# Optimization experiments

Measured on AMD Instinct MI355X. Metric: run time of the kernel, lower is better.

## Reference

```python
import jax, jax.numpy as jnp
import numpy as np

EPS = 1e-5


def _interp_conv(x, pos_in, pos_out, idx, w1, b1, w2, b2, kernel, bias):
    # x: [B, Cin, Nin]; idx: [Nout, K] neighbor indices into the input grid.
    off = pos_in[idx] - pos_out[:, None, :]            # [Nout, K, 2] relative offsets
    h = jax.nn.relu(off @ w1 + b1)                     # [Nout, K, 16] weight-net hidden
    A = h @ w2 + b2                                    # [Nout, K, T] interp weights onto T kernel taps
    feat = x[:, :, idx]                                # [B, Cin, Nout, K] irregular gather
    taps = jnp.einsum('bcnk,nkt->bcnt', feat, A)       # resample neighbors onto canonical taps
    return jnp.einsum('bcnt,oct->bon', taps, kernel) + bias[None, :, None]


def _bn_relu(x, g, b):
    # BatchNorm1d (training-style batch stats over (B, N)) + ReLU
    m = x.mean(axis=(0, 2), keepdims=True)
    v = x.var(axis=(0, 2), keepdims=True)
    return jax.nn.relu((x - m) * jax.lax.rsqrt(v + EPS) * g[None, :, None] + b[None, :, None])


def setup_inputs():
    key = jax.random.key(0)
    ks = jax.random.split(key, 24)
    B, N1, N2, N3, K, T = 16, 50176, 12544, 3136, 9, 9
    d = {}
    d['x'] = jax.random.normal(ks[0], (B, 3, N1), jnp.float32)
    d['l1'] = jax.random.uniform(ks[1], (N1, 2), jnp.float32)
    d['l2'] = jax.random.uniform(ks[2], (N2, 2), jnp.float32)
    d['l3'] = jax.random.uniform(ks[3], (N3, 2), jnp.float32)
    d['knn1'] = jax.random.randint(ks[4], (N2, K), 0, N1)
    d['knn2'] = jax.random.randint(ks[5], (N2, K), 0, N2)
    d['knn3'] = jax.random.randint(ks[6], (N2, K), 0, N2)
    d['pool_idx'] = jax.random.randint(ks[7], (N3, 4), 0, N2)
    cins = {'c1': 3, 'c2': 32, 'c3': 32}
    couts = {'c1': 32, 'c2': 32, 'c3': 64}
    for i, p in enumerate(['c1', 'c2', 'c3']):
        d[p + '_wn_w1'] = jax.random.normal(ks[8 + 4 * i], (2, 16), jnp.float32) * 0.5
        d[p + '_wn_b1'] = jnp.zeros(16, jnp.float32)
        d[p + '_wn_w2'] = jax.random.normal(ks[9 + 4 * i], (16, T), jnp.float32) * 0.3
        d[p + '_wn_b2'] = jnp.zeros(T, jnp.float32)
        d[p + '_kernel'] = jax.random.normal(ks[10 + 4 * i], (couts[p], cins[p], T), jnp.float32) * np.float32(1.0 / np.sqrt(cins[p] * T))
        d[p + '_bias'] = jnp.zeros(couts[p], jnp.float32)
    for p, c in [('bn1', 32), ('bn2', 32), ('bn3', 64)]:
        d[p + '_g'] = jnp.ones(c, jnp.float32)
        d[p + '_b'] = jnp.zeros(c, jnp.float32)
    return d


def reference(x, l1, l2, l3, knn1, knn2, knn3, pool_idx,
              c1_wn_w1, c1_wn_b1, c1_wn_w2, c1_wn_b2, c1_kernel, c1_bias,
              c2_wn_w1, c2_wn_b1, c2_wn_w2, c2_wn_b2, c2_kernel, c2_bias,
              c3_wn_w1, c3_wn_b1, c3_wn_w2, c3_wn_b2, c3_kernel, c3_bias,
              bn1_g, bn1_b, bn2_g, bn2_b, bn3_g, bn3_b):
    h = _interp_conv(x, l1, l2, knn1, c1_wn_w1, c1_wn_b1, c1_wn_w2, c1_wn_b2, c1_kernel, c1_bias)
    h = _bn_relu(h, bn1_g, bn1_b)
    h = _interp_conv(h, l2, l2, knn2, c2_wn_w1, c2_wn_b1, c2_wn_w2, c2_wn_b2, c2_kernel, c2_bias)
    h = _bn_relu(h, bn2_g, bn2_b)
    h = _interp_conv(h, l2, l2, knn3, c3_wn_w1, c3_wn_b1, c3_wn_w2, c3_wn_b2, c3_kernel, c3_bias)
    h = _bn_relu(h, bn3_g, bn3_b)
    # MaxPoolNG: max over 4 nearest neighbors on the non-uniform grid -> [B, 64, N3]
    return h[:, :, pool_idx].max(axis=-1)
```

## Files before the change

### kernel.cpp

```cpp
#include <hip/hip_runtime.h>
#include <hip/hip_bf16.h>
#include <cfloat>

#define N1C 50176
#define N2C 12544
#define N3C 3136

typedef __attribute__((ext_vector_type(8))) short short8v;
typedef __attribute__((ext_vector_type(4))) float f32x4;

static __device__ __forceinline__ unsigned short f2bf(float f){
  __hip_bfloat16 h = __float2bfloat16(f);
  return *reinterpret_cast<unsigned short*>(&h);
}
static __device__ __forceinline__ float bflo(unsigned v){
  return __uint_as_float(v << 16);
}
static __device__ __forceinline__ float bfhi(unsigned v){
  return __uint_as_float(v & 0xFFFF0000u);
}
static __device__ __forceinline__ float bf2f(unsigned short u){
  return __uint_as_float(((unsigned)u) << 16);
}
static __device__ __forceinline__ unsigned pk2(float a, float b){
  return (unsigned)f2bf(a) | ((unsigned)f2bf(b) << 16);
}
static __device__ __forceinline__ short8v pack8(f32x4 L, f32x4 H){
  short8v r;
  r[0]=(short)f2bf(L[0]); r[1]=(short)f2bf(L[1]); r[2]=(short)f2bf(L[2]); r[3]=(short)f2bf(L[3]);
  r[4]=(short)f2bf(H[0]); r[5]=(short)f2bf(H[1]); r[6]=(short)f2bf(H[2]); r[7]=(short)f2bf(H[3]);
  return r;
}

__global__ __launch_bounds__(256) void transpose_x_kernel(
    const float* __restrict__ x, unsigned short* __restrict__ xTb)
{
  __shared__ float tile[48][65];
  int n0 = blockIdx.x * 64;
  int tid = threadIdx.x;
  int i = tid & 63;
  for (int rr = tid >> 6; rr < 48; rr += 4)
    tile[rr][i] = x[(size_t)rr * N1C + n0 + i];
  __syncthreads();
  for (int j = tid; j < 64*64; j += 256){
    int ii = j >> 6, bc = j & 63, b = bc >> 2, c = bc & 3;
    float v = (c < 3) ? tile[b*3 + c][ii] : 0.f;
    xTb[(size_t)n0 * 64 + j] = f2bf(v);
  }
}

__global__ __launch_bounds__(256) void compute_A_kernel(
    const float* __restrict__ pos_in, const float* __restrict__ pos_out,
    const int* __restrict__ idx,
    const float* __restrict__ w1, const float* __restrict__ b1,
    const float* __restrict__ w2, const float* __restrict__ b2,
    float* __restrict__ Abuf)
{
  int g = blockIdx.x * 256 + threadIdx.x;
  if (g >= N2C * 9) return;
  int n = g / 9;
  int p = idx[g];
  float o0 = pos_in[2*p]   - pos_out[2*n];
  float o1 = pos_in[2*p+1] - pos_out[2*n+1];
  float A[9];
  #pragma unroll
  for (int t = 0; t < 9; t++) A[t] = b2[t];
  #pragma unroll
  for (int j = 0; j < 16; j++){
    float h = fmaxf(fmaf(o0, w1[j], fmaf(o1, w1[16+j], b1[j])), 0.f);
    #pragma unroll
    for (int t = 0; t < 9; t++) A[t] = fmaf(h, w2[j*9 + t], A[t]);
  }
  #pragma unroll
  for (int t = 0; t < 9; t++) Abuf[(size_t)g*9 + t] = A[t];
}

__global__ __launch_bounds__(256) void wcvt_kernel(
    const float* __restrict__ W, unsigned short* __restrict__ Wb,
    int total, int K, int KW, int mode)
{
  int i = blockIdx.x * 256 + threadIdx.x;
  if (i >= total) return;
  int o = i / KW, r = i % KW;
  float v;
  if (mode == 0){
    v = (r < K) ? W[o*K + r] : 0.f;
  } else {
    int t = r >> 5, c = r & 31;
    v = W[o*288 + c*9 + t];
  }
  Wb[i] = f2bf(v);
}

template<int CIN, int CINP, int COUT, int NPB, bool AFFINE>
__global__ __launch_bounds__(256) void conv_mfma_kernel(
    const unsigned short* __restrict__ in, const int* __restrict__ idx,
    const float* __restrict__ Abuf, const unsigned short* __restrict__ Wb,
    const float* __restrict__ bias,
    const float* __restrict__ scale, const float* __restrict__ shift,
    unsigned short* __restrict__ out, float* __restrict__ gpart)
{
  constexpr int K    = CIN * 9;
  constexpr int KW   = (K < 32) ? 32 : K;
  constexpr int KROW = (K < 32) ? 48 : 296;
  constexpr int CHUNKS = KW / 32;
  constexpr int OT   = COUT / 16;
  constexpr int HP   = CINP / 2;
  constexpr int PPT  = 16 * HP;

  __shared__ alignas(16) unsigned short Tb[NPB * 16 * KROW];
  __shared__ float As[NPB * 81];
  __shared__ int   Ip[NPB * 9];
  __shared__ float Sw[4 * COUT];
  __shared__ float Sq[4 * COUT];

  int n0 = blockIdx.x * NPB;
  int tid = threadIdx.x;
  for (int i = tid; i < NPB*81; i += 256) As[i] = Abuf[(size_t)n0*81 + i];
  if (tid < NPB*9) Ip[tid] = idx[n0*9 + tid];
  for (int i = tid; i < 4*COUT; i += 256){ Sw[i] = 0.f; Sq[i] = 0.f; }
  if (K < 32){
    for (int i = tid; i < NPB*16*KROW/2; i += 256) ((unsigned*)Tb)[i] = 0u;
  }
  __syncthreads();

  for (int u = tid; u < NPB*PPT; u += 256){
    int ni = u / PPT, loc = u % PPT;
    int b = loc / HP, c2 = loc % HP;
    const float* As_n = As + ni*81;
    const int*   ip   = Ip + ni*9;
    float scx=1.f, shx=0.f, scy=1.f, shy=0.f;
    if (AFFINE){
      scx = scale[2*c2];   shx = shift[2*c2];
      scy = scale[2*c2+1]; shy = shift[2*c2+1];
    }
    float fx[9], fy[9];
    #pragma unroll
    for (int k = 0; k < 9; k++){
      unsigned v = *(const unsigned*)(in + ((size_t)ip[k]*16 + b)*CINP + 2*c2);
      float x0 = bflo(v), y0 = bfhi(v);
      if (AFFINE){
        x0 = fmaxf(fmaf(x0, scx, shx), 0.f);
        y0 = fmaxf(fmaf(y0, scy, shy), 0.f);
      }
      fx[k] = x0; fy[k] = y0;
    }
    unsigned short e[18];
    #pragma unroll
    for (int t = 0; t < 9; t++){
      float s0 = 0.f, s1 = 0.f;
      #pragma unroll
      for (int k = 0; k < 9; k++){
        float a = As_n[k*9 + t];
        s0 = fmaf(fx[k], a, s0);
        s1 = fmaf(fy[k], a, s1);
      }
      e[t] = f2bf(s0); e[9+t] = f2bf(s1);
    }
    unsigned* dst = (unsigned*)(Tb + (ni*16 + b)*KROW + 18*c2);
    #pragma unroll
    for (int j = 0; j < 9; j++) dst[j] = (unsigned)e[2*j] | ((unsigned)e[2*j+1] << 16);
  }
  __syncthreads();

  int w = tid >> 6, l = tid & 63, lr = l & 15, lg = l >> 4;
  float smr[4] = {0,0,0,0}, sqr[4] = {0,0,0,0};
  int oBase = 0;
  for (int wi = w; wi < NPB*OT; wi += 4){
    int ni = wi / OT, ot = wi % OT;
    oBase = 16*ot + 4*lg;
    f32x4 acc;
    #pragma unroll
    for (int r = 0; r < 4; r++) acc[r] = bias[oBase + r];
    const short8v* ap = (const short8v*)(Wb + (size_t)(16*ot + lr)*KW) + lg;
    const short8v* bp = (const short8v*)(Tb + (ni*16 + lr)*KROW) + lg;
    #pragma unroll
    for (int kk = 0; kk < CHUNKS; kk++)
      acc = __builtin_amdgcn_mfma_f32_16x16x32_bf16(ap[kk*4], bp[kk*4], acc, 0, 0, 0);
    ushort4 o4;
    o4.x = f2bf(acc[0]); o4.y = f2bf(acc[1]); o4.z = f2bf(acc[2]); o4.w = f2bf(acc[3]);
    *(ushort4*)(out + ((size_t)(n0 + ni)*16 + lr)*COUT + oBase) = o4;
    #pragma unroll
    for (int r = 0; r < 4; r++){
      smr[r] += acc[r];
      sqr[r] = fmaf(acc[r], acc[r], sqr[r]);
    }
  }
  #pragma unroll
  for (int m = 1; m < 16; m <<= 1){
    #pragma unroll
    for (int r = 0; r < 4; r++){
      smr[r] += __shfl_xor(smr[r], m);
      sqr[r] += __shfl_xor(sqr[r], m);
    }
  }
  if (lr == 0){
    #pragma unroll
    for (int r = 0; r < 4; r++){
      Sw[w*COUT + oBase + r] = smr[r];
      Sq[w*COUT + oBase + r] = sqr[r];
    }
  }
  __syncthreads();
  for (int o = tid; o < COUT; o += 256){
    float sm = Sw[o] + Sw[COUT + o] + Sw[2*COUT + o] + Sw[3*COUT + o];
    float sq = Sq[o] + Sq[COUT + o] + Sq[2*COUT + o] + Sq[3*COUT + o];
    gpart[(size_t)blockIdx.x * 2*COUT + o] = sm;
    gpart[(size_t)blockIdx.x * 2*COUT + COUT + o] = sq;
  }
}

template<int COUT>
__global__ __launch_bounds__(256, 2) void conv_wave_kernel(
    const unsigned short* __restrict__ in, const int* __restrict__ idx,
    const float* __restrict__ Abuf, const unsigned short* __restrict__ Wb,
    const float* __restrict__ bias,
    const float* __restrict__ scale, const float* __restrict__ shift,
    unsigned short* __restrict__ out, float* __restrict__ gpart)
{
  constexpr int NPB = 4;
  constexpr int OT  = COUT / 16;
  constexpr int USZ = 128;

  __shared__ alignas(16) float U[NPB * USZ];

  int tid = threadIdx.x;
  int w = tid >> 6, l = tid & 63;
  int n0 = blockIdx.x * NPB;
  int nws = __builtin_amdgcn_readfirstlane(n0 + w);

  const float* Ap = Abuf + (size_t)nws * 81;
  float a0 = Ap[l];
  float a1 = (l < 17) ? Ap[64 + l] : 0.f;

  int ip[9];
  {
    const int* ipr = idx + nws * 9;
    #pragma unroll
    for (int k = 0; k < 9; k++) ip[k] = ipr[k];
  }

  int b = l & 15, cg = l >> 4;
  const unsigned short* gbase = in + b*32 + cg*8;
  uint4 rv0 = *(const uint4*)(gbase + (size_t)ip[0]*512);
  uint4 rv1 = *(const uint4*)(gbase + (size_t)ip[1]*512);
  uint4 rv2 = *(const uint4*)(gbase + (size_t)ip[2]*512);
  uint4 rv3 = *(const uint4*)(gbase + (size_t)ip[3]*512);
  uint4 rv4 = *(const uint4*)(gbase + (size_t)ip[4]*512);
  uint4 rv5 = *(const uint4*)(gbase + (size_t)ip[5]*512);
  uint4 rv6 = *(const uint4*)(gbase + (size_t)ip[6]*512);
  uint4 rv7 = *(const uint4*)(gbase + (size_t)ip[7]*512);
  uint4 rv8 = *(const uint4*)(gbase + (size_t)ip[8]*512);
  float4 scLf = *(const float4*)(scale + cg*8);
  float4 scHf = *(const float4*)(scale + cg*8 + 4);
  float4 shLf = *(const float4*)(shift + cg*8);
  float4 shHf = *(const float4*)(shift + cg*8 + 4);
  __builtin_amdgcn_sched_barrier(0);

  float* Aw = U + w * USZ;
  {
    int k = l / 9, t = l - k*9;
    Aw[k*12 + t] = a0;
    if (l < 17){
      int j = l + 64;
      int k2 = j / 9, t2 = j - k2*9;
      Aw[k2*12 + t2] = a1;
    }
  }

  f32x4 scL; scL[0]=scLf.x; scL[1]=scLf.y; scL[2]=scLf.z; scL[3]=scLf.w;
  f32x4 shL; shL[0]=shLf.x; shL[1]=shLf.y; shL[2]=shLf.z; shL[3]=shLf.w;
  f32x4 scH; scH[0]=scHf.x; scH[1]=scHf.y; scH[2]=scHf.z; scH[3]=scHf.w;
  f32x4 shH; shH[0]=shHf.x; shH[1]=shHf.y; shH[2]=shHf.z; shH[3]=shHf.w;

  f32x4 tL0={0,0,0,0},tL1={0,0,0,0},tL2={0,0,0,0},tL3={0,0,0,0},tL4={0,0,0,0},
        tL5={0,0,0,0},tL6={0,0,0,0},tL7={0,0,0,0},tL8={0,0,0,0};
  f32x4 tH0={0,0,0,0},tH1={0,0,0,0},tH2={0,0,0,0},tH3={0,0,0,0},tH4={0,0,0,0},
        tH5={0,0,0,0},tH6={0,0,0,0},tH7={0,0,0,0},tH8={0,0,0,0};

#define KSTEP(RV, K) { \
    f32x4 fL_, fH_; \
    fL_[0]=bflo(RV.x); fL_[1]=bfhi(RV.x); fL_[2]=bflo(RV.y); fL_[3]=bfhi(RV.y); \
    fH_[0]=bflo(RV.z); fH_[1]=bfhi(RV.z); fH_[2]=bflo(RV.w); fH_[3]=bfhi(RV.w); \
    fL_ = fL_ * scL + shL; fH_ = fH_ * scH + shH; \
    fL_[0]=fmaxf(fL_[0],0.f); fL_[1]=fmaxf(fL_[1],0.f); \
    fL_[2]=fmaxf(fL_[2],0.f); fL_[3]=fmaxf(fL_[3],0.f); \
    fH_[0]=fmaxf(fH_[0],0.f); fH_[1]=fmaxf(fH_[1],0.f); \
    fH_[2]=fmaxf(fH_[2],0.f); fH_[3]=fmaxf(fH_[3],0.f); \
    f32x4 a03_ = *(const f32x4*)(Aw + (K)*12); \
    f32x4 a47_ = *(const f32x4*)(Aw + (K)*12 + 4); \
    float a8_ = Aw[(K)*12 + 8]; \
    tL0 += fL_ * a03_[0]; tH0 += fH_ * a03_[0]; \
    tL1 += fL_ * a03_[1]; tH1 += fH_ * a03_[1]; \
    tL2 += fL_ * a03_[2]; tH2 += fH_ * a03_[2]; \
    tL3 += fL_ * a03_[3]; tH3 += fH_ * a03_[3]; \
    tL4 += fL_ * a47_[0]; tH4 += fH_ * a47_[0]; \
    tL5 += fL_ * a47_[1]; tH5 += fH_ * a47_[1]; \
    tL6 += fL_ * a47_[2]; tH6 += fH_ * a47_[2]; \
    tL7 += fL_ * a47_[3]; tH7 += fH_ * a47_[3]; \
    tL8 += fL_ * a8_;     tH8 += fH_ * a8_; }

  KSTEP(rv0,0) KSTEP(rv1,1) KSTEP(rv2,2) KSTEP(rv3,3) KSTEP(rv4,4)
  KSTEP(rv5,5) KSTEP(rv6,6) KSTEP(rv7,7) KSTEP(rv8,8)
#undef KSTEP

  short8v fr0 = pack8(tL0, tH0);
  short8v fr1 = pack8(tL1, tH1);
  short8v fr2 = pack8(tL2, tH2);
  short8v fr3 = pack8(tL3, tH3);
  short8v fr4 = pack8(tL4, tH4);
  short8v fr5 = pack8(tL5, tH5);
  short8v fr6 = pack8(tL6, tH6);
  short8v fr7 = pack8(tL7, tH7);
  short8v fr8 = pack8(tL8, tH8);

  f32x4 sm0={0,0,0,0}, sm1={0,0,0,0}, sm2={0,0,0,0}, sm3={0,0,0,0};
  f32x4 sq0={0,0,0,0}, sq1={0,0,0,0}, sq2={0,0,0,0}, sq3={0,0,0,0};
  #pragma unroll
  for (int ot = 0; ot < OT; ot++){
    int oBase = 16*ot + 4*cg;
    f32x4 a3;
    a3[0]=bias[oBase]; a3[1]=bias[oBase+1]; a3[2]=bias[oBase+2]; a3[3]=bias[oBase+3];
    const short8v* ap = (const short8v*)(Wb + (size_t)(16*ot + b)*288) + cg;
    a3 = __builtin_amdgcn_mfma_f32_16x16x32_bf16(ap[0],  fr0, a3, 0, 0, 0);
    a3 = __builtin_amdgcn_mfma_f32_16x16x32_bf16(ap[4],  fr1, a3, 0, 0, 0);
    a3 = __builtin_amdgcn_mfma_f32_16x16x32_bf16(ap[8],  fr2, a3, 0, 0, 0);
    a3 = __builtin_amdgcn_mfma_f32_16x16x32_bf16(ap[12], fr3, a3, 0, 0, 0);
    a3 = __builtin_amdgcn_mfma_f32_16x16x32_bf16(ap[16], fr4, a3, 0, 0, 0);
    a3 = __builtin_amdgcn_mfma_f32_16x16x32_bf16(ap[20], fr5, a3, 0, 0, 0);
    a3 = __builtin_amdgcn_mfma_f32_16x16x32_bf16(ap[24], fr6, a3, 0, 0, 0);
    a3 = __builtin_amdgcn_mfma_f32_16x16x32_bf16(ap[28], fr7, a3, 0, 0, 0);
    a3 = __builtin_amdgcn_mfma_f32_16x16x32_bf16(ap[32], fr8, a3, 0, 0, 0);
    ushort4 o4;
    o4.x = f2bf(a3[0]); o4.y = f2bf(a3[1]); o4.z = f2bf(a3[2]); o4.w = f2bf(a3[3]);
    *(ushort4*)(out + ((size_t)nws*16 + b)*COUT + oBase) = o4;
    if (ot==0){ sm0 += a3; sq0 += a3*a3; }
    else if (ot==1){ sm1 += a3; sq1 += a3*a3; }
    else if (ot==2){ sm2 += a3; sq2 += a3*a3; }
    else { sm3 += a3; sq3 += a3*a3; }
  }

  #pragma unroll
  for (int ot = 0; ot < OT; ot++){
    f32x4 s = (ot==0) ? sm0 : ((ot==1) ? sm1 : ((ot==2) ? sm2 : sm3));
    f32x4 q = (ot==0) ? sq0 : ((ot==1) ? sq1 : ((ot==2) ? sq2 : sq3));
    #pragma unroll
    for (int m = 1; m < 16; m <<= 1){
      #pragma unroll
      for (int r = 0; r < 4; r++){
        s[r] += __shfl_xor(s[r], m);
        q[r] += __shfl_xor(q[r], m);
      }
    }
    if (b == 0){
      int oBase = 16*ot + 4*cg;
      #pragma unroll
      for (int r = 0; r < 4; r++){
        U[w*USZ + oBase + r]        = s[r];
        U[w*USZ + COUT + oBase + r] = q[r];
      }
    }
  }
  __syncthreads();
  for (int o = tid; o < COUT; o += 256){
    float smv = U[o] + U[USZ + o] + U[2*USZ + o] + U[3*USZ + o];
    float sqv = U[COUT + o] + U[USZ + COUT + o] + U[2*USZ + COUT + o] + U[3*USZ + COUT + o];
    gpart[(size_t)blockIdx.x * 2*COUT + o] = smv;
    gpart[(size_t)blockIdx.x * 2*COUT + COUT + o] = sqv;
  }
}

__global__ __launch_bounds__(256) void bn_finalize_kernel(
    const float* __restrict__ gpart, int NB, int C,
    const float* __restrict__ g, const float* __restrict__ bb,
    float* __restrict__ sc, float* __restrict__ sh, float invN)
{
  int c = blockIdx.x;
  float sm = 0.f, sq = 0.f;
  for (int i = threadIdx.x; i < NB; i += 256){
    sm += gpart[(size_t)i*2*C + c];
    sq += gpart[(size_t)i*2*C + C + c];
  }
  #pragma unroll
  for (int off = 32; off > 0; off >>= 1){
    sm += __shfl_down(sm, off);
    sq += __shfl_down(sq, off);
  }
  __shared__ float rs[8];
  int wd = threadIdx.x >> 6, ln = threadIdx.x & 63;
  if (ln == 0){ rs[wd] = sm; rs[4+wd] = sq; }
  __syncthreads();
  if (threadIdx.x == 0){
    float S = rs[0]+rs[1]+rs[2]+rs[3], Q = rs[4]+rs[5]+rs[6]+rs[7];
    float mean = S * invN;
    float var  = fmaxf(Q * invN - mean*mean, 0.f);
    float s = g[c] * rsqrtf(var + 1e-5f);
    sc[c] = s;
    sh[c] = bb[c] - mean * s;
  }
}

__global__ __launch_bounds__(256) void pool_kernel(
    const unsigned short* __restrict__ h3, const int* __restrict__ pidx,
    const float* __restrict__ sc, const float* __restrict__ sh,
    float* __restrict__ out)
{
  __shared__ float P[16][1024];
  int m0 = blockIdx.x * 16;
  int tid = threadIdx.x;
  for (int mi = 0; mi < 16; mi++){
    int m = m0 + mi;
    int p0 = pidx[m*4+0], p1 = pidx[m*4+1], p2 = pidx[m*4+2], p3 = pidx[m*4+3];
    #pragma unroll
    for (int q = 0; q < 4; q++){
      int bo = tid + q*256;
      int o = bo & 63;
      float s = sc[o], h = sh[o];
      float v0 = fmaf(bf2f(h3[(size_t)p0*1024 + bo]), s, h);
      float v1 = fmaf(bf2f(h3[(size_t)p1*1024 + bo]), s, h);
      float v2 = fmaf(bf2f(h3[(size_t)p2*1024 + bo]), s, h);
      float v3 = fmaf(bf2f(h3[(size_t)p3*1024 + bo]), s, h);
      P[mi][bo] = fmaxf(fmaxf(fmaxf(v0,v1), fmaxf(v2,v3)), 0.f);
    }
  }
  __syncthreads();
  #pragma unroll
  for (int w = 0; w < 4; w++){
    int r = tid + w*256;
    float* dst = out + (size_t)r*N3C + m0;
    #pragma unroll
    for (int mi = 0; mi < 16; mi++) dst[mi] = P[mi][r];
  }
}

extern "C" void kernel_launch(void* const* d_in, const int* in_sizes, int n_in,
                              void* d_out, int out_size, void* d_ws, size_t ws_size,
                              hipStream_t stream)
{
  const float* x    = (const float*)d_in[0];
  const float* l1   = (const float*)d_in[1];
  const float* l2   = (const float*)d_in[2];
  const int* knn1   = (const int*)d_in[4];
  const int* knn2   = (const int*)d_in[5];
  const int* knn3   = (const int*)d_in[6];
  const int* pidx   = (const int*)d_in[7];

  const float* c1_w1 = (const float*)d_in[8];
  const float* c1_b1 = (const float*)d_in[9];
  const float* c1_w2 = (const float*)d_in[10];
  const float* c1_b2 = (const float*)d_in[11];
  const float* c1_k  = (const float*)d_in[12];
  const float* c1_bs = (const float*)d_in[13];
  const float* c2_w1 = (const float*)d_in[14];
  const float* c2_b1 = (const float*)d_in[15];
  const float* c2_w2 = (const float*)d_in[16];
  const float* c2_b2 = (const float*)d_in[17];
  const float* c2_k  = (const float*)d_in[18];
  const float* c2_bs = (const float*)d_in[19];
  const float* c3_w1 = (const float*)d_in[20];
  const float* c3_b1 = (const float*)d_in[21];
  const float* c3_w2 = (const float*)d_in[22];
  const float* c3_b2 = (const float*)d_in[23];
  const float* c3_k  = (const float*)d_in[24];
  const float* c3_bs = (const float*)d_in[25];
  const float* bn1_g = (const float*)d_in[26];
  const float* bn1_b = (const float*)d_in[27];
  const float* bn2_g = (const float*)d_in[28];
  const float* bn2_b = (const float*)d_in[29];
  const float* bn3_g = (const float*)d_in[30];
  const float* bn3_b = (const float*)d_in[31];

  char* ws = (char*)d_ws;
  unsigned short* xTb = (unsigned short*)(ws + 0);
  unsigned short* h1  = (unsigned short*)(ws + 6422528);
  unsigned short* h2  = (unsigned short*)(ws + 19267584);
  unsigned short* h3  = (unsigned short*)(ws + 32112640);
  float* Abuf         = (float*)(ws + 57802752);
  float* gpart        = (float*)(ws + 61867008);
  unsigned short* wb1 = (unsigned short*)(ws + 65078272);
  unsigned short* wb2 = (unsigned short*)(ws + 65081344);
  unsigned short* wb3 = (unsigned short*)(ws + 65099776);
  float* sc1 = (float*)(ws + 65137664); float* sh1 = sc1 + 32;
  float* sc2 = sh1 + 32;                float* sh2 = sc2 + 32;
  float* sc3 = sh2 + 32;                float* sh3 = sc3 + 64;

  const float invN = 1.0f / (float)(N2C * 16);
  const int ablocks = (N2C * 9 + 255) / 256;

  transpose_x_kernel<<<N1C/64, 256, 0, stream>>>(x, xTb);
  wcvt_kernel<<<(32*32 + 255)/256, 256, 0, stream>>>(c1_k, wb1, 32*32, 27, 32, 0);
  wcvt_kernel<<<(32*288 + 255)/256, 256, 0, stream>>>(c2_k, wb2, 32*288, 288, 288, 1);
  wcvt_kernel<<<(64*288 + 255)/256, 256, 0, stream>>>(c3_k, wb3, 64*288, 288, 288, 1);

  compute_A_kernel<<<ablocks, 256, 0, stream>>>(l1, l2, knn1, c1_w1, c1_b1, c1_w2, c1_b2, Abuf);
  conv_mfma_kernel<3, 4, 32, 8, false><<<N2C/8, 256, 0, stream>>>(
      xTb, knn1, Abuf, wb1, c1_bs, nullptr, nullptr, h1, gpart);
  bn_finalize_kernel<<<32, 256, 0, stream>>>(gpart, N2C/8, 32, bn1_g, bn1_b, sc1, sh1, invN);

  compute_A_kernel<<<ablocks, 256, 0, stream>>>(l2, l2, knn2, c2_w1, c2_b1, c2_w2, c2_b2, Abuf);
  conv_wave_kernel<32><<<N2C/4, 256, 0, stream>>>(
      h1, knn2, Abuf, wb2, c2_bs, sc1, sh1, h2, gpart);
  bn_finalize_kernel<<<32, 256, 0, stream>>>(gpart, N2C/4, 32, bn2_g, bn2_b, sc2, sh2, invN);

  compute_A_kernel<<<ablocks, 256, 0, stream>>>(l2, l2, knn3, c3_w1, c3_b1, c3_w2, c3_b2, Abuf);
  conv_wave_kernel<64><<<N2C/4, 256, 0, stream>>>(
      h2, knn3, Abuf, wb3, c3_bs, sc2, sh2, h3, gpart);
  bn_finalize_kernel<<<64, 256, 0, stream>>>(gpart, N2C/4, 64, bn3_g, bn3_b, sc3, sh3, invN);

  pool_kernel<<<N3C/16, 256, 0, stream>>>(h3, pidx, sc3, sh3, (float*)d_out);
}
```

Measured before the change: 171.1 us.

## Process four points per wave with software-pipelined gathers and LDS-staged weights

Each wave now handles four output points instead of one. The neighbor gather and A-weight loads for the next point are issued before the MFMA/stat stage of the current point, hiding gather latency. Conv weights are copied once per block into LDS with a padded row stride instead of being read from global per MFMA. This raises register and LDS use per block and cuts the block count by four, which may lower occupancy.

```diff
diff --git a/kernel.cpp b/kernel.cpp
--- a/kernel.cpp
+++ b/kernel.cpp
@@ -210,73 +210,25 @@
   }
 }
 
-template<int COUT>
-__global__ __launch_bounds__(256, 2) void conv_wave_kernel(
-    const unsigned short* __restrict__ in, const int* __restrict__ idx,
-    const float* __restrict__ Abuf, const unsigned short* __restrict__ Wb,
-    const float* __restrict__ bias,
-    const float* __restrict__ scale, const float* __restrict__ shift,
-    unsigned short* __restrict__ out, float* __restrict__ gpart)
-{
-  constexpr int NPB = 4;
-  constexpr int OT  = COUT / 16;
-  constexpr int USZ = 128;
-
-  __shared__ alignas(16) float U[NPB * USZ];
-
-  int tid = threadIdx.x;
-  int w = tid >> 6, l = tid & 63;
-  int n0 = blockIdx.x * NPB;
-  int nws = __builtin_amdgcn_readfirstlane(n0 + w);
-
-  const float* Ap = Abuf + (size_t)nws * 81;
-  float a0 = Ap[l];
-  float a1 = (l < 17) ? Ap[64 + l] : 0.f;
-
-  int ip[9];
-  {
-    const int* ipr = idx + nws * 9;
-    #pragma unroll
-    for (int k = 0; k < 9; k++) ip[k] = ipr[k];
-  }
-
-  int b = l & 15, cg = l >> 4;
-  const unsigned short* gbase = in + b*32 + cg*8;
-  uint4 rv0 = *(const uint4*)(gbase + (size_t)ip[0]*512);
-  uint4 rv1 = *(const uint4*)(gbase + (size_t)ip[1]*512);
-  uint4 rv2 = *(const uint4*)(gbase + (size_t)ip[2]*512);
-  uint4 rv3 = *(const uint4*)(gbase + (size_t)ip[3]*512);
-  uint4 rv4 = *(const uint4*)(gbase + (size_t)ip[4]*512);
-  uint4 rv5 = *(const uint4*)(gbase + (size_t)ip[5]*512);
-  uint4 rv6 = *(const uint4*)(gbase + (size_t)ip[6]*512);
-  uint4 rv7 = *(const uint4*)(gbase + (size_t)ip[7]*512);
-  uint4 rv8 = *(const uint4*)(gbase + (size_t)ip[8]*512);
-  float4 scLf = *(const float4*)(scale + cg*8);
-  float4 scHf = *(const float4*)(scale + cg*8 + 4);
-  float4 shLf = *(const float4*)(shift + cg*8);
-  float4 shHf = *(const float4*)(shift + cg*8 + 4);
-  __builtin_amdgcn_sched_barrier(0);
-
-  float* Aw = U + w * USZ;
-  {
-    int k = l / 9, t = l - k*9;
-    Aw[k*12 + t] = a0;
-    if (l < 17){
-      int j = l + 64;
-      int k2 = j / 9, t2 = j - k2*9;
-      Aw[k2*12 + t2] = a1;
-    }
-  }
-
-  f32x4 scL; scL[0]=scLf.x; scL[1]=scLf.y; scL[2]=scLf.z; scL[3]=scLf.w;
-  f32x4 shL; shL[0]=shLf.x; shL[1]=shLf.y; shL[2]=shLf.z; shL[3]=shLf.w;
-  f32x4 scH; scH[0]=scHf.x; scH[1]=scHf.y; scH[2]=scHf.z; scH[3]=scHf.w;
-  f32x4 shH; shH[0]=shHf.x; shH[1]=shHf.y; shH[2]=shHf.z; shH[3]=shHf.w;
-
-  f32x4 tL0={0,0,0,0},tL1={0,0,0,0},tL2={0,0,0,0},tL3={0,0,0,0},tL4={0,0,0,0},
-        tL5={0,0,0,0},tL6={0,0,0,0},tL7={0,0,0,0},tL8={0,0,0,0};
-  f32x4 tH0={0,0,0,0},tH1={0,0,0,0},tH2={0,0,0,0},tH3={0,0,0,0},tH4={0,0,0,0},
-        tH5={0,0,0,0},tH6={0,0,0,0},tH7={0,0,0,0},tH8={0,0,0,0};
+
+#define PREFETCH(NWSN) { \
+    const float* Ap_ = Abuf + (size_t)(NWSN)*81; \
+    a0 = Ap_[l]; a1 = (l < 17) ? Ap_[64 + l] : 0.f; \
+    const int* ipr_ = idx + (size_t)(NWSN)*9; \
+    int i0_=ipr_[0], i1_=ipr_[1], i2_=ipr_[2], i3_=ipr_[3], i4_=ipr_[4], \
+        i5_=ipr_[5], i6_=ipr_[6], i7_=ipr_[7], i8_=ipr_[8]; \
+    rv0 = *(const uint4*)(gbase + (size_t)i0_*512); \
+    rv1 = *(const uint4*)(gbase + (size_t)i1_*512); \
+    rv2 = *(const uint4*)(gbase + (size_t)i2_*512); \
+    rv3 = *(const uint4*)(gbase + (size_t)i3_*512); \
+    rv4 = *(const uint4*)(gbase + (size_t)i4_*512); \
+    rv5 = *(const uint4*)(gbase + (size_t)i5_*512); \
+    rv6 = *(const uint4*)(gbase + (size_t)i6_*512); \
+    rv7 = *(const uint4*)(gbase + (size_t)i7_*512); \
+    rv8 = *(const uint4*)(gbase + (size_t)i8_*512); }
+
+#define AWRITE { int k_ = l/9, t_ = l - k_*9; Aw[k_*12 + t_] = a0; \
+    if (l < 17){ int j_ = l + 64; int k2_ = j_/9, t2_ = j_ - k2_*9; Aw[k2_*12 + t2_] = a1; } }
 
 #define KSTEP(RV, K) { \
     f32x4 fL_, fH_; \
@@ -300,45 +252,115 @@
     tL7 += fL_ * a47_[3]; tH7 += fH_ * a47_[3]; \
     tL8 += fL_ * a8_;     tH8 += fH_ * a8_; }
 
-  KSTEP(rv0,0) KSTEP(rv1,1) KSTEP(rv2,2) KSTEP(rv3,3) KSTEP(rv4,4)
-  KSTEP(rv5,5) KSTEP(rv6,6) KSTEP(rv7,7) KSTEP(rv8,8)
-#undef KSTEP
-
-  short8v fr0 = pack8(tL0, tH0);
-  short8v fr1 = pack8(tL1, tH1);
-  short8v fr2 = pack8(tL2, tH2);
-  short8v fr3 = pack8(tL3, tH3);
-  short8v fr4 = pack8(tL4, tH4);
-  short8v fr5 = pack8(tL5, tH5);
-  short8v fr6 = pack8(tL6, tH6);
-  short8v fr7 = pack8(tL7, tH7);
-  short8v fr8 = pack8(tL8, tH8);
+#define TAPS_AND_PACK { \
+    f32x4 tL0={0,0,0,0},tL1={0,0,0,0},tL2={0,0,0,0},tL3={0,0,0,0},tL4={0,0,0,0}, \
+          tL5={0,0,0,0},tL6={0,0,0,0},tL7={0,0,0,0},tL8={0,0,0,0}; \
+    f32x4 tH0={0,0,0,0},tH1={0,0,0,0},tH2={0,0,0,0},tH3={0,0,0,0},tH4={0,0,0,0}, \
+          tH5={0,0,0,0},tH6={0,0,0,0},tH7={0,0,0,0},tH8={0,0,0,0}; \
+    KSTEP(rv0,0) KSTEP(rv1,1) KSTEP(rv2,2) KSTEP(rv3,3) KSTEP(rv4,4) \
+    KSTEP(rv5,5) KSTEP(rv6,6) KSTEP(rv7,7) KSTEP(rv8,8) \
+    fr0 = pack8(tL0,tH0); fr1 = pack8(tL1,tH1); fr2 = pack8(tL2,tH2); \
+    fr3 = pack8(tL3,tH3); fr4 = pack8(tL4,tH4); fr5 = pack8(tL5,tH5); \
+    fr6 = pack8(tL6,tH6); fr7 = pack8(tL7,tH7); fr8 = pack8(tL8,tH8); }
+
+#define MFMA_STATS(NWSC) { \
+    _Pragma("unroll") \
+    for (int ot = 0; ot < OT; ot++){ \
+      int oBase = 16*ot + 4*cg; \
+      f32x4 a3; \
+      a3[0]=bias[oBase]; a3[1]=bias[oBase+1]; a3[2]=bias[oBase+2]; a3[3]=bias[oBase+3]; \
+      const short8v* ap_ = (const short8v*)(Wl + (size_t)(16*ot + b)*WROW) + cg; \
+      a3 = __builtin_amdgcn_mfma_f32_16x16x32_bf16(ap_[0],  fr0, a3, 0, 0, 0); \
+      a3 = __builtin_amdgcn_mfma_f32_16x16x32_bf16(ap_[4],  fr1, a3, 0, 0, 0); \
+      a3 = __builtin_amdgcn_mfma_f32_16x16x32_bf16(ap_[8],  fr2, a3, 0, 0, 0); \
+      a3 = __builtin_amdgcn_mfma_f32_16x16x32_bf16(ap_[12], fr3, a3, 0, 0, 0); \
+      a3 = __builtin_amdgcn_mfma_f32_16x16x32_bf16(ap_[16], fr4, a3, 0, 0, 0); \
+      a3 = __builtin_amdgcn_mfma_f32_16x16x32_bf16(ap_[20], fr5, a3, 0, 0, 0); \
+      a3 = __builtin_amdgcn_mfma_f32_16x16x32_bf16(ap_[24], fr6, a3, 0, 0, 0); \
+      a3 = __builtin_amdgcn_mfma_f32_16x16x32_bf16(ap_[28], fr7, a3, 0, 0, 0); \
+      a3 = __builtin_amdgcn_mfma_f32_16x16x32_bf16(ap_[32], fr8, a3, 0, 0, 0); \
+      ushort4 o4_; \
+      o4_.x = f2bf(a3[0]); o4_.y = f2bf(a3[1]); o4_.z = f2bf(a3[2]); o4_.w = f2bf(a3[3]); \
+      *(ushort4*)(out + ((size_t)(NWSC)*16 + b)*COUT + oBase) = o4_; \
+      if (ot==0){ sm0 += a3; sq0 += a3*a3; } \
+      else if (ot==1){ sm1 += a3; sq1 += a3*a3; } \
+      else if (ot==2){ sm2 += a3; sq2 += a3*a3; } \
+      else { sm3 += a3; sq3 += a3*a3; } } }
+
+template<int COUT>
+__global__ __launch_bounds__(256, 2) void conv_wave_kernel(
+    const unsigned short* __restrict__ in, const int* __restrict__ idx,
+    const float* __restrict__ Abuf, const unsigned short* __restrict__ Wb,
+    const float* __restrict__ bias,
+    const float* __restrict__ scale, const float* __restrict__ shift,
+    unsigned short* __restrict__ out, float* __restrict__ gpart)
+{
+  constexpr int NPB  = 4;
+  constexpr int PPW  = 4;
+  constexpr int OT   = COUT / 16;
+  constexpr int WROW = 296;
+  constexpr int USZ  = 128;
+
+  __shared__ alignas(16) unsigned short Wl[COUT * WROW];
+  __shared__ alignas(16) float U[NPB * USZ];
+
+  int tid = threadIdx.x;
+  int w = tid >> 6, l = tid & 63;
+  int base = blockIdx.x * (NPB*PPW) + w * PPW;
+  int b = l & 15, cg = l >> 4;
+
+  for (int j = tid; j < COUT*36; j += 256){
+    int o = j / 36, c = j % 36;
+    *(uint4*)(Wl + (size_t)o*WROW + c*8) = *(const uint4*)(Wb + (size_t)o*288 + c*8);
+  }
+
+  const unsigned short* gbase = in + b*32 + cg*8;
+  float* Aw = U + w * USZ;
+
+  float4 scLf = *(const float4*)(scale + cg*8);
+  float4 scHf = *(const float4*)(scale + cg*8 + 4);
+  float4 shLf = *(const float4*)(shift + cg*8);
+  float4 shHf = *(const float4*)(shift + cg*8 + 4);
+  f32x4 scL; scL[0]=scLf.x; scL[1]=scLf.y; scL[2]=scLf.z; scL[3]=scLf.w;
+  f32x4 shL; shL[0]=shLf.x; shL[1]=shLf.y; shL[2]=shLf.z; shL[3]=shLf.w;
+  f32x4 scH; scH[0]=scHf.x; scH[1]=scHf.y; scH[2]=scHf.z; scH[3]=scHf.w;
+  f32x4 shH; shH[0]=shHf.x; shH[1]=shHf.y; shH[2]=shHf.z; shH[3]=shHf.w;
+
+  __syncthreads();
 
   f32x4 sm0={0,0,0,0}, sm1={0,0,0,0}, sm2={0,0,0,0}, sm3={0,0,0,0};
   f32x4 sq0={0,0,0,0}, sq1={0,0,0,0}, sq2={0,0,0,0}, sq3={0,0,0,0};
-  #pragma unroll
-  for (int ot = 0; ot < OT; ot++){
-    int oBase = 16*ot + 4*cg;
-    f32x4 a3;
-    a3[0]=bias[oBase]; a3[1]=bias[oBase+1]; a3[2]=bias[oBase+2]; a3[3]=bias[oBase+3];
-    const short8v* ap = (const short8v*)(Wb + (size_t)(16*ot + b)*288) + cg;
-    a3 = __builtin_amdgcn_mfma_f32_16x16x32_bf16(ap[0],  fr0, a3, 0, 0, 0);
-    a3 = __builtin_amdgcn_mfma_f32_16x16x32_bf16(ap[4],  fr1, a3, 0, 0, 0);
-    a3 = __builtin_amdgcn_mfma_f32_16x16x32_bf16(ap[8],  fr2, a3, 0, 0, 0);
-    a3 = __builtin_amdgcn_mfma_f32_16x16x32_bf16(ap[12], fr3, a3, 0, 0, 0);
-    a3 = __builtin_amdgcn_mfma_f32_16x16x32_bf16(ap[16], fr4, a3, 0, 0, 0);
-    a3 = __builtin_amdgcn_mfma_f32_16x16x32_bf16(ap[20], fr5, a3, 0, 0, 0);
-    a3 = __builtin_amdgcn_mfma_f32_16x16x32_bf16(ap[24], fr6, a3, 0, 0, 0);
-    a3 = __builtin_amdgcn_mfma_f32_16x16x32_bf16(ap[28], fr7, a3, 0, 0, 0);
-    a3 = __builtin_amdgcn_mfma_f32_16x16x32_bf16(ap[32], fr8, a3, 0, 0, 0);
-    ushort4 o4;
-    o4.x = f2bf(a3[0]); o4.y = f2bf(a3[1]); o4.z = f2bf(a3[2]); o4.w = f2bf(a3[3]);
-    *(ushort4*)(out + ((size_t)nws*16 + b)*COUT + oBase) = o4;
-    if (ot==0){ sm0 += a3; sq0 += a3*a3; }
-    else if (ot==1){ sm1 += a3; sq1 += a3*a3; }
-    else if (ot==2){ sm2 += a3; sq2 += a3*a3; }
-    else { sm3 += a3; sq3 += a3*a3; }
-  }
+  uint4 rv0,rv1,rv2,rv3,rv4,rv5,rv6,rv7,rv8;
+  short8v fr0,fr1,fr2,fr3,fr4,fr5,fr6,fr7,fr8;
+  float a0, a1;
+
+  int nws0 = __builtin_amdgcn_readfirstlane(base + 0);
+  PREFETCH(nws0);
+  AWRITE;
+
+  TAPS_AND_PACK;
+  int nws1 = __builtin_amdgcn_readfirstlane(base + 1);
+  PREFETCH(nws1);
+  __builtin_amdgcn_sched_barrier(0);
+  MFMA_STATS(nws0);
+  AWRITE;
+
+  TAPS_AND_PACK;
+  int nws2 = __builtin_amdgcn_readfirstlane(base + 2);
+  PREFETCH(nws2);
+  __builtin_amdgcn_sched_barrier(0);
+  MFMA_STATS(nws1);
+  AWRITE;
+
+  TAPS_AND_PACK;
+  int nws3 = __builtin_amdgcn_readfirstlane(base + 3);
+  PREFETCH(nws3);
+  __builtin_amdgcn_sched_barrier(0);
+  MFMA_STATS(nws2);
+  AWRITE;
+
+  TAPS_AND_PACK;
+  MFMA_STATS(nws3);
 
   #pragma unroll
   for (int ot = 0; ot < OT; ot++){
@@ -369,6 +391,12 @@
     gpart[(size_t)blockIdx.x * 2*COUT + COUT + o] = sqv;
   }
 }
+
+#undef PREFETCH
+#undef AWRITE
+#undef KSTEP
+#undef TAPS_AND_PACK
+#undef MFMA_STATS
 
 __global__ __launch_bounds__(256) void bn_finalize_kernel(
     const float* __restrict__ gpart, int NB, int C,
@@ -486,6 +514,7 @@
 
   const float invN = 1.0f / (float)(N2C * 16);
   const int ablocks = (N2C * 9 + 255) / 256;
+  const int cwblocks = N2C / 16;
 
   transpose_x_kernel<<<N1C/64, 256, 0, stream>>>(x, xTb);
   wcvt_kernel<<<(32*32 + 255)/256, 256, 0, stream>>>(c1_k, wb1, 32*32, 27, 32, 0);
@@ -498,14 +527,14 @@
   bn_finalize_kernel<<<32, 256, 0, stream>>>(gpart, N2C/8, 32, bn1_g, bn1_b, sc1, sh1, invN);
 
   compute_A_kernel<<<ablocks, 256, 0, stream>>>(l2, l2, knn2, c2_w1, c2_b1, c2_w2, c2_b2, Abuf);
-  conv_wave_kernel<32><<<N2C/4, 256, 0, stream>>>(
+  conv_wave_kernel<32><<<cwblocks, 256, 0, stream>>>(
       h1, knn2, Abuf, wb2, c2_bs, sc1, sh1, h2, gpart);
-  bn_finalize_kernel<<<32, 256, 0, stream>>>(gpart, N2C/4, 32, bn2_g, bn2_b, sc2, sh2, invN);
+  bn_finalize_kernel<<<32, 256, 0, stream>>>(gpart, cwblocks, 32, bn2_g, bn2_b, sc2, sh2, invN);
 
   compute_A_kernel<<<ablocks, 256, 0, stream>>>(l2, l2, knn3, c3_w1, c3_b1, c3_w2, c3_b2, Abuf);
-  conv_wave_kernel<64><<<N2C/4, 256, 0, stream>>>(
+  conv_wave_kernel<64><<<cwblocks, 256, 0, stream>>>(
       h2, knn3, Abuf, wb3, c3_bs, sc2, sh2, h3, gpart);
-  bn_finalize_kernel<<<64, 256, 0, stream>>>(gpart, N2C/4, 64, bn3_g, bn3_b, sc3, sh3, invN);
+  bn_finalize_kernel<<<64, 256, 0, stream>>>(gpart, cwblocks, 64, bn3_g, bn3_b, sc3, sh3, invN);
 
   pool_kernel<<<N3C/16, 256, 0, stream>>>(h3, pidx, sc3, sh3, (float*)d_out);
 }
```

Result: faster. 142.5 us (-16.7%).
